# Kernel tuning notes

Hardware: AMD Instinct MI355X
Metric: run time of the kernel (lower is better)

The kernel has to match this reference:

```python
import math
import jax, jax.numpy as jnp
import numpy as np

LOCAL_CONTEXT = 128
B, T, H, E = 1, 1024, 8, 64
NB_ROWS = 64  # projection rows; cosh features -> m = 2*NB_ROWS = 128


def softmax_kernel(data, projection, is_query, softmax_temp):
    """Scatterbrain Performer softmax kernel with cosh features, eps=0.
    data: (B,H,N,E), projection: (R,E). Returns (prime (B,H,N,2R), log_scale).
    log_scale is (B,H,N,1) for queries, (B,H,1,1) for keys."""
    data_normalizer = math.sqrt(softmax_temp)
    ratio = (2 * projection.shape[0]) ** -0.5
    data_dash = jnp.einsum('bhne,re->bhnr', data_normalizer * data, projection)
    diag = 0.5 * (data_normalizer ** 2) * jnp.sum(data * data, axis=-1, keepdims=True)
    log_vals = jnp.concatenate([data_dash, -data_dash], axis=-1) - diag  # (B,H,N,2R)
    axes = (-1,) if is_query else (-1, -2)
    stab = jax.lax.stop_gradient(jnp.max(log_vals, axis=axes, keepdims=True))
    prime = ratio * jnp.exp(log_vals - stab)
    return prime, stab


def setup_inputs() -> dict:
    key = jax.random.key(0)
    k1, k2, k3, k4 = jax.random.split(key, 4)
    return {
        'query': jax.random.normal(k1, (B, T, H, E), dtype=jnp.float32),
        'key': jax.random.normal(k2, (B, T, H, E), dtype=jnp.float32),
        'value': jax.random.normal(k3, (B, T, H, E), dtype=jnp.float32),
        'projection': jax.random.normal(k4, (NB_ROWS, E), dtype=jnp.float32),
    }


def reference(query, key, value, projection):
    Bq, Tq, Hq, Eq = query.shape
    S = key.shape[1]
    w = LOCAL_CONTEXT
    temp = 1.0 / math.sqrt(Eq)

    q = jnp.transpose(query, (0, 2, 1, 3))  # (B,H,T,E)
    k = jnp.transpose(key, (0, 2, 1, 3))    # (B,H,S,E)
    v = jnp.transpose(value, (0, 2, 1, 3))  # (B,H,S,D)

    q_prime, q_ls = softmax_kernel(q, projection, True, temp)   # (B,H,T,m), (B,H,T,1)
    k_prime, k_ls = softmax_kernel(k, projection, False, temp)  # (B,H,S,m), (B,H,1,1)
    prime_log_scale = q_ls + k_ls  # (B,H,T,1)

    # global (Performer) linear attention pieces
    qk1 = jnp.einsum('bhtm,bhm->bht', q_prime, jnp.sum(k_prime, axis=2))
    kv = jnp.einsum('bhsm,bhsd->bhmd', k_prime, v)
    qkv = jnp.einsum('bhtm,bhmd->bhtd', q_prime, kv)

    # banded local window: query i attends keys [i - w//2, i - w//2 + w)
    i = jnp.arange(Tq)[:, None]
    j = jnp.arange(w)[None, :]
    idx = i - w // 2 + j              # (T,w)
    valid = (idx >= 0) & (idx < S)
    idx_c = jnp.clip(idx, 0, S - 1)

    k_g = k[:, :, idx_c, :]           # (B,H,T,w,E)
    QK = temp * jnp.einsum('bhte,bhtwe->bhtw', q, k_g)
    QK = jnp.where(valid, QK, -jnp.inf)

    kp_g = k_prime[:, :, idx_c, :]    # (B,H,T,w,m)
    dots_prime = jnp.einsum('bhtm,bhtwm->bhtw', q_prime, kp_g)
    dots_prime = jnp.where(valid, dots_prime, 0.0)

    QK_lse = jax.scipy.special.logsumexp(QK, axis=-1, keepdims=True)
    dp_sum = jnp.sum(dots_prime, axis=-1, keepdims=True)
    lr_log_norm = jnp.log(jnp.clip(qk1[..., None] - dp_sum, 1e-24, None)) + prime_log_scale
    log_norm = jnp.logaddexp(QK_lse, lr_log_norm)  # (B,H,T,1)

    prime_scale = jnp.exp(prime_log_scale - log_norm)
    attn_local = jnp.exp(QK - log_norm) - dots_prime * prime_scale  # (B,H,T,w)

    v_g = v[:, :, idx_c, :]           # (B,H,T,w,D)
    out_local = jnp.einsum('bhtw,bhtwd->bhtd', attn_local, v_g)
    out = out_local + qkv * prime_scale
    return jnp.transpose(out, (0, 2, 1, 3))  # (B,T,H,E)
```

## Files before the change

### kernel.cpp

```cpp
#include <hip/hip_runtime.h>
#include <hip/hip_bf16.h>
#include <math.h>

#define DN     0.35355339059327373f
#define RATIO  0.08838834764831845f
#define TEMP   0.125f
#define KLS    8.0f

typedef short s16x8 __attribute__((ext_vector_type(8)));
typedef float f32x4 __attribute__((ext_vector_type(4)));

static __device__ __forceinline__ ushort f2bf(float f) {
    __hip_bfloat16 h = __float2bfloat16(f);
    return *reinterpret_cast<ushort*>(&h);
}
static __device__ __forceinline__ float bf2f(ushort u) {
    __hip_bfloat16 h = *reinterpret_cast<__hip_bfloat16*>(&u);
    return __bfloat162float(h);
}
static __device__ __forceinline__ s16x8 pack8(const ushort* u) {
    union { s16x8 v; ushort u[8]; } P;
#pragma unroll
    for (int i = 0; i < 8; ++i) P.u[i] = u[i];
    return P.v;
}
static __device__ __forceinline__ float load8_split(const float* p, s16x8& ho, s16x8& lo) {
    f32x4 a = *(const f32x4*)p;
    f32x4 b = *(const f32x4*)(p + 4);
    float v[8] = {a.x, a.y, a.z, a.w, b.x, b.y, b.z, b.w};
    ushort hu[8], lu[8];
    float ss = 0.f;
#pragma unroll
    for (int i = 0; i < 8; ++i) {
        ss += v[i] * v[i];
        hu[i] = f2bf(v[i]);
        lu[i] = f2bf(v[i] - bf2f(hu[i]));
    }
    ho = pack8(hu); lo = pack8(lu);
    return ss;
}

#define MFMA(a, b, c) __builtin_amdgcn_mfma_f32_16x16x32_bf16(a, b, c, 0, 0, 0)

__global__ __launch_bounds__(256) void feat_kernel(const float* __restrict__ qin,
    const float* __restrict__ kin, const float* __restrict__ vin,
    const float* __restrict__ proj,
    ushort* __restrict__ qh, ushort* __restrict__ qph, float* __restrict__ qls,
    ushort* __restrict__ kh, ushort* __restrict__ kph,
    ushort* __restrict__ vT, float* __restrict__ pkv, float* __restrict__ pksum)
{
    __shared__ float v_lds[32][65];
    __shared__ float p_lds[32][133];
    __shared__ float diag_lds[32];
    __shared__ float ad_part[4][32];
    __shared__ float ad_lds[32];
    int tid = threadIdx.x;
    int bid = blockIdx.x;
    int h = bid & 7, rest = bid >> 3;
    int isq = rest >> 5;
    int c = rest & 31, s0 = c * 32;
    int w = tid >> 6, lane = tid & 63, l15 = lane & 15, lk = lane >> 4;
    const float* din = isq ? qin : kin;
    ushort* xh = isq ? qh : kh;

    if (!isq) {
#pragma unroll
        for (int i = 0; i < 8; ++i) {
            int f = tid + 256 * i;
            int sl = f >> 6, e = f & 63;
            v_lds[sl][e] = vin[((size_t)((s0 + sl) * 8 + h) << 6) + e];
        }
    }

    s16x8 ah[2][2], al[2][2];
    float qq[2] = {0.f, 0.f};
#pragma unroll
    for (int mt = 0; mt < 2; ++mt)
#pragma unroll
        for (int kt = 0; kt < 2; ++kt) {
            size_t goff = ((size_t)((s0 + mt * 16 + l15) * 8 + h) << 6) + kt * 32 + lk * 8;
            qq[mt] += load8_split(din + goff, ah[mt][kt], al[mt][kt]);
            if (w == mt * 2 + kt)
                *(s16x8*)(xh + goff) = ah[mt][kt];
        }
    if (w == 0) {
#pragma unroll
        for (int mt = 0; mt < 2; ++mt) {
            float s = qq[mt];
            s += __shfl_xor(s, 16, 64);
            s += __shfl_xor(s, 32, 64);
            if (lk == 0) diag_lds[mt * 16 + l15] = 0.0625f * s;
        }
    }
    f32x4 dacc[2] = {{0,0,0,0},{0,0,0,0}};
#pragma unroll
    for (int kt = 0; kt < 2; ++kt) {
        s16x8 bh, bl;
        load8_split(proj + ((w * 16 + l15) << 6) + kt * 32 + lk * 8, bh, bl);
#pragma unroll
        for (int mt = 0; mt < 2; ++mt) {
            dacc[mt] = MFMA(ah[mt][kt], bh, dacc[mt]);
            dacc[mt] = MFMA(ah[mt][kt], bl, dacc[mt]);
            dacc[mt] = MFMA(al[mt][kt], bh, dacc[mt]);
        }
    }

    if (isq) {
#pragma unroll
        for (int mt = 0; mt < 2; ++mt)
#pragma unroll
            for (int j = 0; j < 4; ++j) {
                float rm = fabsf(DN * dacc[mt][j]);
#pragma unroll
                for (int m = 1; m < 16; m <<= 1) rm = fmaxf(rm, __shfl_xor(rm, m, 16));
                if (l15 == 0) ad_part[w][mt * 16 + lk * 4 + j] = rm;
            }
        __syncthreads();
        if (tid < 32) {
            float ad = fmaxf(fmaxf(ad_part[0][tid], ad_part[1][tid]),
                             fmaxf(ad_part[2][tid], ad_part[3][tid]));
            ad_lds[tid] = ad;
            qls[(size_t)((s0 + tid) * 8 + h)] = ad - diag_lds[tid];
        }
        __syncthreads();
#pragma unroll
        for (int mt = 0; mt < 2; ++mt)
#pragma unroll
            for (int j = 0; j < 4; ++j) {
                int t = mt * 16 + lk * 4 + j;
                int r = w * 16 + l15;
                float dash = DN * dacc[mt][j];
                float ad = ad_lds[t];
                p_lds[t][r]      = RATIO * __expf( dash - ad);
                p_lds[t][64 + r] = RATIO * __expf(-dash - ad);
            }
    } else {
        __syncthreads();
#pragma unroll
        for (int mt = 0; mt < 2; ++mt)
#pragma unroll
            for (int j = 0; j < 4; ++j) {
                int t = mt * 16 + lk * 4 + j;
                int r = w * 16 + l15;
                float dash = DN * dacc[mt][j];
                float cc = diag_lds[t] + KLS;
                p_lds[t][r]      = RATIO * __expf( dash - cc);
                p_lds[t][64 + r] = RATIO * __expf(-dash - cc);
            }
#pragma unroll
        for (int j = 0; j < 8; ++j) {
            int o = tid + 256 * j;
            int d = o >> 5, sidx = o & 31;
            vT[((size_t)(h * 64 + d) << 10) + s0 + sidx] = f2bf(v_lds[sidx][d]);
        }
    }
    __syncthreads();

    ushort* ph = isq ? qph : kph;
#pragma unroll
    for (int i = 0; i < 16; ++i) {
        int o = tid + 256 * i;
        int sl = o >> 7, m = o & 127;
        size_t goff = ((size_t)((s0 + sl) * 8 + h) << 7) + m;
        ph[goff] = f2bf(p_lds[sl][m]);
    }
    if (!isq) {
        if (tid < 128) {
            float s = 0.f;
#pragma unroll
            for (int sl = 0; sl < 32; ++sl) s += p_lds[sl][tid];
            pksum[(h * 32 + c) * 128 + tid] = s;
        }
        s16x8 bv;
        {
            ushort tmp[8];
#pragma unroll
            for (int i = 0; i < 8; ++i) tmp[i] = f2bf(v_lds[lk * 8 + i][w * 16 + l15]);
            bv = pack8(tmp);
        }
        float* pkvb = pkv + ((size_t)(h * 32 + c) << 13);
        int d = w * 16 + l15;
#pragma unroll
        for (int mt = 0; mt < 8; ++mt) {
            ushort tmp[8];
#pragma unroll
            for (int i = 0; i < 8; ++i) tmp[i] = f2bf(p_lds[lk * 8 + i][mt * 16 + l15]);
            s16x8 a = pack8(tmp);
            f32x4 acc = {0, 0, 0, 0};
            acc = MFMA(a, bv, acc);
            *(f32x4*)(pkvb + d * 128 + mt * 16 + lk * 4) = acc;
        }
    }
}

__global__ __launch_bounds__(256) void kvred_kernel(const float* __restrict__ pkv,
    const float* __restrict__ pksum, ushort* __restrict__ kvT, float* __restrict__ ksum)
{
    int tid = threadIdx.x;
    int h = blockIdx.x & 7, dg = blockIdx.x >> 3;
    int dd = tid >> 7, m = tid & 127;
    int d = dg * 2 + dd;
    float s = 0.f;
#pragma unroll
    for (int c = 0; c < 32; ++c)
        s += pkv[((size_t)(h * 32 + c) << 13) + d * 128 + m];
    kvT[((size_t)(h * 64 + d) << 7) + m] = f2bf(s);
    if (dg == 0 && tid < 128) {
        float ks = 0.f;
#pragma unroll
        for (int c = 0; c < 32; ++c) ks += pksum[(h * 32 + c) * 128 + tid];
        ksum[h * 128 + tid] = ks;
    }
}

__global__ __launch_bounds__(256) void main_kernel(
    const ushort* __restrict__ qh, const ushort* __restrict__ qph,
    const float* __restrict__ qls,
    const ushort* __restrict__ kh, const ushort* __restrict__ kph,
    const ushort* __restrict__ vT, const ushort* __restrict__ kvT,
    const float* __restrict__ ksum, float* __restrict__ outp)
{
    __shared__ float QKb[16][152];
    __shared__ float DPb[16][152];
    __shared__ ushort ATb[16][168];
    __shared__ float qk1s[16], plss[16], lns[16], pss[16];

    int tid = threadIdx.x;
    int h = blockIdx.x & 7, t0 = (blockIdx.x >> 3) << 4;
    int w = tid >> 6, lane = tid & 63, l15 = lane & 15, lk = lane >> 4;
    int tl = tid >> 4, sub = tid & 15;

    int dcol = w * 16 + l15;
    s16x8 bkv[4];
    {
        const ushort* kvTrow = kvT + ((size_t)(h * 64 + dcol) << 7);
#pragma unroll
        for (int kt = 0; kt < 4; ++kt)
            bkv[kt] = *(const s16x8*)(kvTrow + kt * 32 + lk * 8);
    }

    s16x8 aqh[2], aph[4];
    {
        int tg = (t0 + l15) * 8 + h;
#pragma unroll
        for (int kt = 0; kt < 2; ++kt)
            aqh[kt] = *(const s16x8*)(qh + ((size_t)tg << 6) + kt * 32 + lk * 8);
#pragma unroll
        for (int kt = 0; kt < 4; ++kt)
            aph[kt] = *(const s16x8*)(qph + ((size_t)tg << 7) + kt * 32 + lk * 8);
    }

    {
        int gid = (t0 + tl) * 8 + h;
        const ushort* ph = qph + ((size_t)gid << 7) + sub * 8;
        const float* ksp = ksum + h * 128 + sub * 8;
        float s = 0.f;
#pragma unroll
        for (int i = 0; i < 8; ++i) s += bf2f(ph[i]) * ksp[i];
#pragma unroll
        for (int m = 1; m < 16; m <<= 1) s += __shfl_xor(s, m, 16);
        if (sub == 0) qk1s[tl] = s;
        if (sub == 1) plss[tl] = qls[gid] + KLS;
    }

    for (int nt = w; nt < 9; nt += 4) {
        int srow = min(max(t0 - 64 + nt * 16 + l15, 0), 1023);
        size_t kbase = ((size_t)(srow * 8 + h)) << 6;
        size_t pbase = ((size_t)(srow * 8 + h)) << 7;
        s16x8 bkh[2], bph[4];
#pragma unroll
        for (int kt = 0; kt < 2; ++kt)
            bkh[kt] = *(const s16x8*)(kh + kbase + kt * 32 + lk * 8);
#pragma unroll
        for (int kt = 0; kt < 4; ++kt)
            bph[kt] = *(const s16x8*)(kph + pbase + kt * 32 + lk * 8);
        f32x4 aqk = {0,0,0,0}, adp = {0,0,0,0};
#pragma unroll
        for (int kt = 0; kt < 2; ++kt)
            aqk = MFMA(aqh[kt], bkh[kt], aqk);
#pragma unroll
        for (int kt = 0; kt < 4; ++kt)
            adp = MFMA(aph[kt], bph[kt], adp);
#pragma unroll
        for (int r = 0; r < 4; ++r) {
            int row = lk * 4 + r, cs = nt * 16 + l15;
            QKb[row][cs] = TEMP * aqk[r];
            DPb[row][cs] = adp[r];
        }
    }
    __syncthreads();

    int clo = max(tl, 64 - t0);
    int chi = min(tl + 128, 1088 - t0);
    float mx = -1e30f, dsum = 0.f;
#pragma unroll
    for (int kk = 0; kk < 9; ++kk) {
        int cs = sub + 16 * kk;
        if (cs >= clo && cs < chi) {
            mx = fmaxf(mx, QKb[tl][cs]);
            dsum += DPb[tl][cs];
        }
    }
#pragma unroll
    for (int m = 1; m < 16; m <<= 1) {
        mx = fmaxf(mx, __shfl_xor(mx, m, 16));
        dsum += __shfl_xor(dsum, m, 16);
    }
    float se = 0.f;
#pragma unroll
    for (int kk = 0; kk < 9; ++kk) {
        int cs = sub + 16 * kk;
        if (cs >= clo && cs < chi) se += __expf(QKb[tl][cs] - mx);
    }
#pragma unroll
    for (int m = 1; m < 16; m <<= 1) se += __shfl_xor(se, m, 16);
    if (sub == 0) {
        float lse = mx + __logf(se);
        float lr = __logf(fmaxf(qk1s[tl] - dsum, 1e-24f)) + plss[tl];
        float mab = fmaxf(lse, lr);
        float ln = mab + log1pf(__expf(fminf(lse, lr) - mab));
        lns[tl] = ln;
        pss[tl] = __expf(plss[tl] - ln);
    }
    __syncthreads();

    {
        float ln = lns[tl], ps = pss[tl];
#pragma unroll
        for (int kk = 0; kk < 10; ++kk) {
            int cs = sub + 16 * kk;
            float att = 0.f;
            if (kk < 9 && cs >= clo && cs < chi)
                att = __expf(QKb[tl][cs] - ln) - DPb[tl][cs] * ps;
            ATb[tl][cs] = f2bf(att);
        }
    }
    __syncthreads();

    f32x4 acc1 = {0,0,0,0}, acc2 = {0,0,0,0};
    const ushort* vTrow = vT + ((size_t)(h * 64 + dcol) << 10);
#pragma unroll
    for (int kt = 0; kt < 5; ++kt) {
        s16x8 a = *(const s16x8*)&ATb[l15][kt * 32 + lk * 8];
        int sc = t0 - 64 + kt * 32 + lk * 8;
        sc = min(max(sc, 0), 1016);
        s16x8 b = *(const s16x8*)(vTrow + sc);
        acc1 = MFMA(a, b, acc1);
    }
#pragma unroll
    for (int kt = 0; kt < 4; ++kt)
        acc2 = MFMA(aph[kt], bkv[kt], acc2);
#pragma unroll
    for (int r = 0; r < 4; ++r) {
        int row = lk * 4 + r;
        float val = acc1[r] + pss[row] * acc2[r];
        outp[((size_t)((t0 + row) * 8 + h) << 6) + dcol] = val;
    }
}

extern "C" void kernel_launch(void* const* d_in, const int* in_sizes, int n_in,
                              void* d_out, int out_size, void* d_ws, size_t ws_size,
                              hipStream_t stream) {
    const float* q    = (const float*)d_in[0];
    const float* kk   = (const float*)d_in[1];
    const float* vv   = (const float*)d_in[2];
    const float* proj = (const float*)d_in[3];
    float* out = (float*)d_out;
    float* ws  = (float*)d_ws;

    ushort* qh    = (ushort*)(ws);
    ushort* qph   = (ushort*)(ws + 262144);
    float*  qls   = ws + 786432;
    ushort* kh    = (ushort*)(ws + 794624);
    ushort* kph   = (ushort*)(ws + 1056768);
    ushort* vT    = (ushort*)(ws + 1581056);
    ushort* kvT   = (ushort*)(ws + 1843200);
    float*  ksum  = ws + 1875968;
    float*  pksum = ws + 1876992;
    float*  pkv   = ws + 1909760;

    feat_kernel<<<512, 256, 0, stream>>>(q, kk, vv, proj, qh, qph, qls,
                                         kh, kph, vT, pkv, pksum);
    kvred_kernel<<<256, 256, 0, stream>>>(pkv, pksum, kvT, ksum);
    main_kernel<<<512, 256, 0, stream>>>(qh, qph, qls, kh, kph,
                                         vT, kvT, ksum, out);
}
```

Before: 25.70 us.

## Widen main kernel to 512 threads and vectorize feature stores

The main kernel now runs 8 waves per block instead of 4. The score tiles are spread across more waves, row reductions use 32-lane groups, and the local-attention MFMA and the global kv MFMA run on separate wave halves, joined through a shared-memory buffer. Separately, the feature kernel writes the bf16 prime features as 16-byte vector stores instead of scalar 2-byte stores. The aim is more parallelism per block and fewer store instructions, at the cost of an extra barrier, extra LDS, and waves that sit idle in some phases.

```diff
diff --git a/kernel.cpp b/kernel.cpp
--- a/kernel.cpp
+++ b/kernel.cpp
@@ -158,11 +158,14 @@
 
     ushort* ph = isq ? qph : kph;
 #pragma unroll
-    for (int i = 0; i < 16; ++i) {
+    for (int i = 0; i < 2; ++i) {
         int o = tid + 256 * i;
-        int sl = o >> 7, m = o & 127;
-        size_t goff = ((size_t)((s0 + sl) * 8 + h) << 7) + m;
-        ph[goff] = f2bf(p_lds[sl][m]);
+        int sl = o >> 4;
+        int mc = (o & 15) * 8;
+        ushort tmp[8];
+#pragma unroll
+        for (int j = 0; j < 8; ++j) tmp[j] = f2bf(p_lds[sl][mc + j]);
+        *(s16x8*)(ph + ((size_t)((s0 + sl) * 8 + h) << 7) + mc) = pack8(tmp);
     }
     if (!isq) {
         if (tid < 128) {
@@ -213,7 +216,7 @@
     }
 }
 
-__global__ __launch_bounds__(256) void main_kernel(
+__global__ __launch_bounds__(512) void main_kernel(
     const ushort* __restrict__ qh, const ushort* __restrict__ qph,
     const float* __restrict__ qls,
     const ushort* __restrict__ kh, const ushort* __restrict__ kph,
@@ -223,21 +226,15 @@
     __shared__ float QKb[16][152];
     __shared__ float DPb[16][152];
     __shared__ ushort ATb[16][168];
+    __shared__ float acc2b[16][68];
     __shared__ float qk1s[16], plss[16], lns[16], pss[16];
 
     int tid = threadIdx.x;
     int h = blockIdx.x & 7, t0 = (blockIdx.x >> 3) << 4;
-    int w = tid >> 6, lane = tid & 63, l15 = lane & 15, lk = lane >> 4;
-    int tl = tid >> 4, sub = tid & 15;
-
-    int dcol = w * 16 + l15;
-    s16x8 bkv[4];
-    {
-        const ushort* kvTrow = kvT + ((size_t)(h * 64 + dcol) << 7);
-#pragma unroll
-        for (int kt = 0; kt < 4; ++kt)
-            bkv[kt] = *(const s16x8*)(kvTrow + kt * 32 + lk * 8);
-    }
+    int w8 = tid >> 6, lane = tid & 63, l15 = lane & 15, lk = lane >> 4;
+    int tl = tid >> 5, sub = tid & 31;
+    int q4 = w8 & 3;
+    int dcol = q4 * 16 + l15;
 
     s16x8 aqh[2], aph[4];
     {
@@ -249,21 +246,28 @@
         for (int kt = 0; kt < 4; ++kt)
             aph[kt] = *(const s16x8*)(qph + ((size_t)tg << 7) + kt * 32 + lk * 8);
     }
+    s16x8 bkv[4];
+    if (w8 >= 4) {
+        const ushort* kvTrow = kvT + ((size_t)(h * 64 + dcol) << 7);
+#pragma unroll
+        for (int kt = 0; kt < 4; ++kt)
+            bkv[kt] = *(const s16x8*)(kvTrow + kt * 32 + lk * 8);
+    }
 
     {
         int gid = (t0 + tl) * 8 + h;
-        const ushort* ph = qph + ((size_t)gid << 7) + sub * 8;
-        const float* ksp = ksum + h * 128 + sub * 8;
+        const ushort* ph = qph + ((size_t)gid << 7) + sub * 4;
+        const float* ksp = ksum + h * 128 + sub * 4;
         float s = 0.f;
 #pragma unroll
-        for (int i = 0; i < 8; ++i) s += bf2f(ph[i]) * ksp[i];
-#pragma unroll
-        for (int m = 1; m < 16; m <<= 1) s += __shfl_xor(s, m, 16);
+        for (int i = 0; i < 4; ++i) s += bf2f(ph[i]) * ksp[i];
+#pragma unroll
+        for (int m = 1; m < 32; m <<= 1) s += __shfl_xor(s, m, 32);
         if (sub == 0) qk1s[tl] = s;
         if (sub == 1) plss[tl] = qls[gid] + KLS;
     }
 
-    for (int nt = w; nt < 9; nt += 4) {
+    for (int nt = w8; nt < 9; nt += 8) {
         int srow = min(max(t0 - 64 + nt * 16 + l15, 0), 1023);
         size_t kbase = ((size_t)(srow * 8 + h)) << 6;
         size_t pbase = ((size_t)(srow * 8 + h)) << 7;
@@ -294,26 +298,26 @@
     int chi = min(tl + 128, 1088 - t0);
     float mx = -1e30f, dsum = 0.f;
 #pragma unroll
-    for (int kk = 0; kk < 9; ++kk) {
-        int cs = sub + 16 * kk;
+    for (int kk = 0; kk < 5; ++kk) {
+        int cs = sub + 32 * kk;
         if (cs >= clo && cs < chi) {
             mx = fmaxf(mx, QKb[tl][cs]);
             dsum += DPb[tl][cs];
         }
     }
 #pragma unroll
-    for (int m = 1; m < 16; m <<= 1) {
-        mx = fmaxf(mx, __shfl_xor(mx, m, 16));
-        dsum += __shfl_xor(dsum, m, 16);
+    for (int m = 1; m < 32; m <<= 1) {
+        mx = fmaxf(mx, __shfl_xor(mx, m, 32));
+        dsum += __shfl_xor(dsum, m, 32);
     }
     float se = 0.f;
 #pragma unroll
-    for (int kk = 0; kk < 9; ++kk) {
-        int cs = sub + 16 * kk;
+    for (int kk = 0; kk < 5; ++kk) {
+        int cs = sub + 32 * kk;
         if (cs >= clo && cs < chi) se += __expf(QKb[tl][cs] - mx);
     }
 #pragma unroll
-    for (int m = 1; m < 16; m <<= 1) se += __shfl_xor(se, m, 16);
+    for (int m = 1; m < 32; m <<= 1) se += __shfl_xor(se, m, 32);
     if (sub == 0) {
         float lse = mx + __logf(se);
         float lr = __logf(fmaxf(qk1s[tl] - dsum, 1e-24f)) + plss[tl];
@@ -327,34 +331,44 @@
     {
         float ln = lns[tl], ps = pss[tl];
 #pragma unroll
-        for (int kk = 0; kk < 10; ++kk) {
-            int cs = sub + 16 * kk;
+        for (int kk = 0; kk < 5; ++kk) {
+            int cs = sub + 32 * kk;
             float att = 0.f;
-            if (kk < 9 && cs >= clo && cs < chi)
+            if (cs >= clo && cs < chi)
                 att = __expf(QKb[tl][cs] - ln) - DPb[tl][cs] * ps;
             ATb[tl][cs] = f2bf(att);
         }
     }
     __syncthreads();
 
-    f32x4 acc1 = {0,0,0,0}, acc2 = {0,0,0,0};
-    const ushort* vTrow = vT + ((size_t)(h * 64 + dcol) << 10);
-#pragma unroll
-    for (int kt = 0; kt < 5; ++kt) {
-        s16x8 a = *(const s16x8*)&ATb[l15][kt * 32 + lk * 8];
-        int sc = t0 - 64 + kt * 32 + lk * 8;
-        sc = min(max(sc, 0), 1016);
-        s16x8 b = *(const s16x8*)(vTrow + sc);
-        acc1 = MFMA(a, b, acc1);
-    }
-#pragma unroll
-    for (int kt = 0; kt < 4; ++kt)
-        acc2 = MFMA(aph[kt], bkv[kt], acc2);
-#pragma unroll
-    for (int r = 0; r < 4; ++r) {
-        int row = lk * 4 + r;
-        float val = acc1[r] + pss[row] * acc2[r];
-        outp[((size_t)((t0 + row) * 8 + h) << 6) + dcol] = val;
+    f32x4 acc1 = {0,0,0,0};
+    if (w8 < 4) {
+        const ushort* vTrow = vT + ((size_t)(h * 64 + dcol) << 10);
+#pragma unroll
+        for (int kt = 0; kt < 5; ++kt) {
+            s16x8 a = *(const s16x8*)&ATb[l15][kt * 32 + lk * 8];
+            int sc = t0 - 64 + kt * 32 + lk * 8;
+            sc = min(max(sc, 0), 1016);
+            s16x8 b = *(const s16x8*)(vTrow + sc);
+            acc1 = MFMA(a, b, acc1);
+        }
+    } else {
+        f32x4 a2 = {0,0,0,0};
+#pragma unroll
+        for (int kt = 0; kt < 4; ++kt)
+            a2 = MFMA(aph[kt], bkv[kt], a2);
+#pragma unroll
+        for (int r = 0; r < 4; ++r)
+            acc2b[lk * 4 + r][dcol] = a2[r];
+    }
+    __syncthreads();
+    if (w8 < 4) {
+#pragma unroll
+        for (int r = 0; r < 4; ++r) {
+            int row = lk * 4 + r;
+            float val = acc1[r] + pss[row] * acc2b[row][dcol];
+            outp[((size_t)((t0 + row) * 8 + h) << 6) + dcol] = val;
+        }
     }
 }
 
@@ -382,6 +396,6 @@
     feat_kernel<<<512, 256, 0, stream>>>(q, kk, vv, proj, qh, qph, qls,
                                          kh, kph, vT, pkv, pksum);
     kvred_kernel<<<256, 256, 0, stream>>>(pkv, pksum, kvT, ksum);
-    main_kernel<<<512, 256, 0, stream>>>(qh, qph, qls, kh, kph,
+    main_kernel<<<512, 512, 0, stream>>>(qh, qph, qls, kh, kph,
                                          vT, kvT, ksum, out);
 }
```

Result: slower. 26.99 us (+5.0%).

## Store partial KV in bf16, vectorize feature stores, split kv reduction

Applied to the files above, without the earlier changes.

Partial KV products are now written and read as bf16 instead of fp32, halving that intermediate traffic between feat_kernel and kvred_kernel. Feature-map stores are vectorized to 16-byte writes per thread instead of scalar ushort stores. The reduction kernel launches twice as many blocks, each handling one d with two halves summed through shared memory. Rounding the partial sums to bf16 before accumulation adds numerical error.

```diff
diff --git a/kernel.cpp b/kernel.cpp
--- a/kernel.cpp
+++ b/kernel.cpp
@@ -8,6 +8,7 @@
 #define KLS    8.0f
 
 typedef short s16x8 __attribute__((ext_vector_type(8)));
+typedef ushort u16x4 __attribute__((ext_vector_type(4)));
 typedef float f32x4 __attribute__((ext_vector_type(4)));
 
 static __device__ __forceinline__ ushort f2bf(float f) {
@@ -47,7 +48,7 @@
     const float* __restrict__ proj,
     ushort* __restrict__ qh, ushort* __restrict__ qph, float* __restrict__ qls,
     ushort* __restrict__ kh, ushort* __restrict__ kph,
-    ushort* __restrict__ vT, float* __restrict__ pkv, float* __restrict__ pksum)
+    ushort* __restrict__ vT, ushort* __restrict__ pkv, float* __restrict__ pksum)
 {
     __shared__ float v_lds[32][65];
     __shared__ float p_lds[32][133];
@@ -158,11 +159,14 @@
 
     ushort* ph = isq ? qph : kph;
 #pragma unroll
-    for (int i = 0; i < 16; ++i) {
+    for (int i = 0; i < 2; ++i) {
         int o = tid + 256 * i;
-        int sl = o >> 7, m = o & 127;
-        size_t goff = ((size_t)((s0 + sl) * 8 + h) << 7) + m;
-        ph[goff] = f2bf(p_lds[sl][m]);
+        int sl = o >> 4;
+        int mc = (o & 15) * 8;
+        ushort tmp[8];
+#pragma unroll
+        for (int j = 0; j < 8; ++j) tmp[j] = f2bf(p_lds[sl][mc + j]);
+        *(s16x8*)(ph + ((size_t)((s0 + sl) * 8 + h) << 7) + mc) = pack8(tmp);
     }
     if (!isq) {
         if (tid < 128) {
@@ -178,7 +182,7 @@
             for (int i = 0; i < 8; ++i) tmp[i] = f2bf(v_lds[lk * 8 + i][w * 16 + l15]);
             bv = pack8(tmp);
         }
-        float* pkvb = pkv + ((size_t)(h * 32 + c) << 13);
+        ushort* pkvb = pkv + ((size_t)(h * 32 + c) << 13);
         int d = w * 16 + l15;
 #pragma unroll
         for (int mt = 0; mt < 8; ++mt) {
@@ -188,24 +192,32 @@
             s16x8 a = pack8(tmp);
             f32x4 acc = {0, 0, 0, 0};
             acc = MFMA(a, bv, acc);
-            *(f32x4*)(pkvb + d * 128 + mt * 16 + lk * 4) = acc;
-        }
-    }
-}
-
-__global__ __launch_bounds__(256) void kvred_kernel(const float* __restrict__ pkv,
+            u16x4 pk;
+#pragma unroll
+            for (int j = 0; j < 4; ++j) pk[j] = f2bf(acc[j]);
+            *(u16x4*)(pkvb + d * 128 + mt * 16 + lk * 4) = pk;
+        }
+    }
+}
+
+__global__ __launch_bounds__(256) void kvred_kernel(const ushort* __restrict__ pkv,
     const float* __restrict__ pksum, ushort* __restrict__ kvT, float* __restrict__ ksum)
 {
+    __shared__ float buf[2][128];
     int tid = threadIdx.x;
-    int h = blockIdx.x & 7, dg = blockIdx.x >> 3;
-    int dd = tid >> 7, m = tid & 127;
-    int d = dg * 2 + dd;
+    int h = blockIdx.x & 7, d = blockIdx.x >> 3;
+    int m = tid & 127, half = tid >> 7;
     float s = 0.f;
 #pragma unroll
-    for (int c = 0; c < 32; ++c)
-        s += pkv[((size_t)(h * 32 + c) << 13) + d * 128 + m];
-    kvT[((size_t)(h * 64 + d) << 7) + m] = f2bf(s);
-    if (dg == 0 && tid < 128) {
+    for (int c = 0; c < 16; ++c) {
+        int cc = half * 16 + c;
+        s += bf2f(pkv[((size_t)(h * 32 + cc) << 13) + d * 128 + m]);
+    }
+    buf[half][m] = s;
+    __syncthreads();
+    if (tid < 128)
+        kvT[((size_t)(h * 64 + d) << 7) + m] = f2bf(buf[0][m] + buf[1][m]);
+    if (blockIdx.x < 8 && tid < 128) {
         float ks = 0.f;
 #pragma unroll
         for (int c = 0; c < 32; ++c) ks += pksum[(h * 32 + c) * 128 + tid];
@@ -377,11 +389,11 @@
     ushort* kvT   = (ushort*)(ws + 1843200);
     float*  ksum  = ws + 1875968;
     float*  pksum = ws + 1876992;
-    float*  pkv   = ws + 1909760;
+    ushort* pkv   = (ushort*)(ws + 1909760);
 
     feat_kernel<<<512, 256, 0, stream>>>(q, kk, vv, proj, qh, qph, qls,
                                          kh, kph, vT, pkv, pksum);
-    kvred_kernel<<<256, 256, 0, stream>>>(pkv, pksum, kvT, ksum);
+    kvred_kernel<<<512, 256, 0, stream>>>(pkv, pksum, kvT, ksum);
     main_kernel<<<512, 256, 0, stream>>>(qh, qph, qls, kh, kph,
                                          vT, kvT, ksum, out);
 }
```

Result: faster. 25.07 us (-2.5%).
